# Optimization experiments

Measured on AMD Instinct MI355X. Metric: run time of the kernel, lower is better.

## Reference

```python
import jax, jax.numpy as jnp
import numpy as np
import math

DIM = 1024
N_HEADS = 16
HEAD_DIM = DIM // N_HEADS


def setup_inputs() -> dict:
    key = jax.random.key(0)
    kx, kk, kq, kv = jax.random.split(key, 4)
    x = jax.random.normal(kx, (4, 2048, DIM), dtype=jnp.float32)
    # torch.rand -> uniform [0,1)
    wk = jax.random.uniform(kk, (N_HEADS, DIM, HEAD_DIM), dtype=jnp.float32)
    wq = jax.random.uniform(kq, (N_HEADS, DIM, HEAD_DIM), dtype=jnp.float32)
    wv = jax.random.uniform(kv, (N_HEADS, DIM, HEAD_DIM), dtype=jnp.float32)
    return {"x": x, "wk": wk, "wq": wq, "wv": wv}


def reference(x, wk, wq, wv):
    # x: [b, l, d]; w*: [n, d, e]
    k = jnp.einsum('bld,nde->bnle', x, wk)
    q = jnp.einsum('bld,nde->bnle', x, wq)
    v = jnp.einsum('bld,nde->bnle', x, wv)
    head_dim = k.shape[-1]
    scores = jnp.einsum('bnle,bnme->bnlm', q, k) / math.sqrt(head_dim)
    s = jax.nn.softmax(scores, axis=-1)
    r = jnp.einsum('bnlm,bnme->blne', s, v)  # [b, l, n, e]
    b, l, n, e = r.shape
    return r.reshape(b, l, n * e)
```

## Files before the change

### kernel.cpp

```cpp
#include <hip/hip_runtime.h>
#include <math.h>

#define DIMX   1024
#define NHEADS 16
#define HD     64
#define BATCH  4
#define SEQ    2048
#define NM     (BATCH * NHEADS * SEQ * HD)

typedef unsigned short ushort_t;
typedef __attribute__((ext_vector_type(8))) short bf16x8;
typedef __attribute__((ext_vector_type(4))) short bf16x4;
typedef __attribute__((ext_vector_type(4))) float f32x4;

#define MFMA16(a, b, c) __builtin_amdgcn_mfma_f32_16x16x32_bf16(a, b, c, 0, 0, 0)

#if __has_builtin(__builtin_amdgcn_mfma_f32_16x16x16bf16_1k)
#define MFMA_PV(a, b, c) __builtin_amdgcn_mfma_f32_16x16x16bf16_1k(a, b, c, 0, 0, 0)
#else
static __device__ __forceinline__ f32x4 mfma_pv_asm(bf16x4 a, bf16x4 b, f32x4 c) {
    asm("v_mfma_f32_16x16x16_bf16 %0, %1, %2, %0" : "+v"(c) : "v"(a), "v"(b));
    return c;
}
#define MFMA_PV(a, b, c) mfma_pv_asm(a, b, c)
#endif

__device__ __forceinline__ ushort_t f2bf(float x) {
    unsigned u = __float_as_uint(x);
    u += 0x7fffu + ((u >> 16) & 1u);
    return (ushort_t)(u >> 16);
}
__device__ __forceinline__ float bf2f(ushort_t h) {
    return __uint_as_float(((unsigned)h) << 16);
}

__device__ __forceinline__ unsigned pack_bf16_trunc(float lo, float hi) {
#if __has_builtin(__builtin_amdgcn_perm)
    return __builtin_amdgcn_perm(__float_as_uint(hi), __float_as_uint(lo), 0x07060302u);
#else
    return (__float_as_uint(lo) >> 16) | (__float_as_uint(hi) & 0xFFFF0000u);
#endif
}
__device__ __forceinline__ float trunc_bf(float x) {
    return __uint_as_float(__float_as_uint(x) & 0xFFFF0000u);
}

__device__ __forceinline__ float fast_exp2(float x) {
#if __has_builtin(__builtin_amdgcn_exp2f)
    return __builtin_amdgcn_exp2f(x);
#else
    return exp2f(x);
#endif
}

#define GLOAD_LDS16(g, l) \
    __builtin_amdgcn_global_load_lds((const __attribute__((address_space(1))) unsigned int*)(g), \
                                     (__attribute__((address_space(3))) unsigned int*)(l), 16, 0, 0)

__global__ __launch_bounds__(256) void convert_x(
    const float* __restrict__ x, ushort_t* __restrict__ Xh, ushort_t* __restrict__ Xl)
{
    int i = blockIdx.x * 256 + threadIdx.x;
    #pragma unroll
    for (int t = 0; t < 4; t++) {
        int idx = t * 524288 + i;
        f32x4 v = ((const f32x4*)x)[idx];
        ushort4 hi, lo;
        hi.x = f2bf(v[0]); lo.x = f2bf(v[0] - bf2f(hi.x));
        hi.y = f2bf(v[1]); lo.y = f2bf(v[1] - bf2f(hi.y));
        hi.z = f2bf(v[2]); lo.z = f2bf(v[2] - bf2f(hi.z));
        hi.w = f2bf(v[3]); lo.w = f2bf(v[3] - bf2f(hi.w));
        ((ushort4*)Xh)[idx] = hi;
        ((ushort4*)Xl)[idx] = lo;
    }
}

__global__ __launch_bounds__(256) void convert_w(
    const float* __restrict__ wk, const float* __restrict__ wq, const float* __restrict__ wv,
    ushort_t* __restrict__ Bqh, ushort_t* __restrict__ Bql, ushort_t* __restrict__ Bvh)
{
    __shared__ float Ts[64][65];
    const int bid = blockIdx.x;
    const int mat = bid >> 8;
    const int rem = bid & 255;
    const int n  = rem >> 4;
    const int dt = rem & 15;
    const float* w = (mat == 0) ? wq : (mat == 1) ? wk : wv;
    const int tid = threadIdx.x;

    #pragma unroll
    for (int t = 0; t < 16; t++) {
        int i = tid + t * 256;
        int r = i >> 6, e = i & 63;
        Ts[r][e] = w[((size_t)n * 1024 + dt * 64 + r) * 64 + e];
    }
    __syncthreads();
    #pragma unroll
    for (int t = 0; t < 16; t++) {
        int i = tid + t * 256;
        int e = i >> 6, r = i & 63;
        float v = Ts[r][e];
        ushort_t hi = f2bf(v);
        size_t o = (size_t)(n * 64 + e) * 1024 + dt * 64 + r;
        if (mat < 2) {
            Bqh[(size_t)mat * 1048576 + o] = hi;
            Bql[(size_t)mat * 1048576 + o] = f2bf(v - bf2f(hi));
        } else {
            Bvh[o] = hi;
        }
    }
}

__global__ __launch_bounds__(256) void proj_qk(
    const ushort_t* __restrict__ Xh, const ushort_t* __restrict__ Xl,
    const ushort_t* __restrict__ Bh, const ushort_t* __restrict__ Bl,
    float* __restrict__ Qf, ushort_t* __restrict__ Khi, ushort_t* __restrict__ Klo)
{
    __shared__ __align__(16) ushort_t Ah[128 * 64];
    __shared__ __align__(16) ushort_t Al[128 * 64];
    __shared__ __align__(16) ushort_t Bhs[128 * 64];
    __shared__ __align__(16) ushort_t Bls[128 * 64];

    const int mt = blockIdx.x, nt = blockIdx.y;
    const int tid = threadIdx.x;
    const int w = tid >> 6, lane = tid & 63, col = lane & 15, quad = lane >> 4;
    const int wm = w & 1, wn = w >> 1;

    f32x4 acc[4][4] = {};

    for (int kc = 0; kc < 1024; kc += 64) {
        __syncthreads();
        #pragma unroll
        for (int i = 0; i < 4; i++) {
            int s = (w * 4 + i) * 64 + lane;
            int r = s >> 3, j = s & 7, g = j ^ (r & 7);
            size_t aoff = (size_t)(mt * 128 + r) * 1024 + kc + g * 8;
            size_t boff = (size_t)(nt * 128 + r) * 1024 + kc + g * 8;
            GLOAD_LDS16(Xh + aoff, Ah  + (size_t)(w * 4 + i) * 512);
            GLOAD_LDS16(Xl + aoff, Al  + (size_t)(w * 4 + i) * 512);
            GLOAD_LDS16(Bh + boff, Bhs + (size_t)(w * 4 + i) * 512);
            GLOAD_LDS16(Bl + boff, Bls + (size_t)(w * 4 + i) * 512);
        }
        __syncthreads();
        #pragma unroll
        for (int kk = 0; kk < 2; kk++) {
            bf16x8 a_h[4], a_l[4], b_h[4], b_l[4];
            const int gi = kk * 4 + quad;
            #pragma unroll
            for (int t = 0; t < 4; t++) {
                int rA = wm * 64 + t * 16 + col;
                int jA = gi ^ (rA & 7);
                a_h[t] = *(const bf16x8*)&Ah[(rA * 8 + jA) * 8];
                a_l[t] = *(const bf16x8*)&Al[(rA * 8 + jA) * 8];
                int rB = wn * 64 + t * 16 + col;
                int jB = gi ^ (rB & 7);
                b_h[t] = *(const bf16x8*)&Bhs[(rB * 8 + jB) * 8];
                b_l[t] = *(const bf16x8*)&Bls[(rB * 8 + jB) * 8];
            }
            #pragma unroll
            for (int t = 0; t < 4; t++)
                #pragma unroll
                for (int u = 0; u < 4; u++) {
                    acc[t][u] = MFMA16(a_h[t], b_h[u], acc[t][u]);
                    acc[t][u] = MFMA16(a_l[t], b_h[u], acc[t][u]);
                    acc[t][u] = MFMA16(a_h[t], b_l[u], acc[t][u]);
                }
        }
    }

    const bool isQ = (nt < 8);
    #pragma unroll
    for (int t = 0; t < 4; t++) {
        #pragma unroll
        for (int u = 0; u < 4; u++) {
            int np = nt * 128 + wn * 64 + u * 16 + col;
            int head = (np >> 6) & 15, e = np & 63;
            #pragma unroll
            for (int rr = 0; rr < 4; rr++) {
                int mm = mt * 128 + wm * 64 + t * 16 + quad * 4 + rr;
                int bi = mm >> 11, l = mm & 2047;
                size_t base = (((size_t)bi * NHEADS + head) * SEQ + l) * HD + e;
                float v = acc[t][u][rr];
                if (isQ) {
                    Qf[base] = v;
                } else {
                    ushort_t hi = f2bf(v);
                    Khi[base] = hi;
                    Klo[base] = f2bf(v - bf2f(hi));
                }
            }
        }
    }
}

__global__ __launch_bounds__(256) void proj_v(
    const ushort_t* __restrict__ Wvh, const ushort_t* __restrict__ Xh,
    ushort_t* __restrict__ Vt)
{
    __shared__ __align__(16) ushort_t Ah[128 * 64];
    __shared__ __align__(16) ushort_t Bhs[128 * 64];

    const int mt = blockIdx.x, nt = blockIdx.y;
    const int tid = threadIdx.x;
    const int w = tid >> 6, lane = tid & 63, col = lane & 15, quad = lane >> 4;
    const int wm = w & 1, wn = w >> 1;

    f32x4 acc[4][4] = {};

    for (int kc = 0; kc < 1024; kc += 64) {
        __syncthreads();
        #pragma unroll
        for (int i = 0; i < 4; i++) {
            int s = (w * 4 + i) * 64 + lane;
            int r = s >> 3, j = s & 7, g = j ^ (r & 7);
            size_t aoff = (size_t)(mt * 128 + r) * 1024 + kc + g * 8;
            size_t boff = (size_t)(nt * 128 + r) * 1024 + kc + g * 8;
            GLOAD_LDS16(Wvh + aoff, Ah  + (size_t)(w * 4 + i) * 512);
            GLOAD_LDS16(Xh  + boff, Bhs + (size_t)(w * 4 + i) * 512);
        }
        __syncthreads();
        #pragma unroll
        for (int kk = 0; kk < 2; kk++) {
            bf16x8 a_h[4], b_h[4];
            const int gi = kk * 4 + quad;
            #pragma unroll
            for (int t = 0; t < 4; t++) {
                int rA = wm * 64 + t * 16 + col;
                a_h[t] = *(const bf16x8*)&Ah[(rA * 8 + (gi ^ (rA & 7))) * 8];
                int rB = wn * 64 + t * 16 + col;
                b_h[t] = *(const bf16x8*)&Bhs[(rB * 8 + (gi ^ (rB & 7))) * 8];
            }
            #pragma unroll
            for (int t = 0; t < 4; t++)
                #pragma unroll
                for (int u = 0; u < 4; u++)
                    acc[t][u] = MFMA16(a_h[t], b_h[u], acc[t][u]);
        }
    }

    #pragma unroll
    for (int t = 0; t < 4; t++) {
        #pragma unroll
        for (int rr = 0; rr < 4; rr++) {
            int ep = mt * 128 + wm * 64 + t * 16 + quad * 4 + rr;
            int head = ep >> 6, e = ep & 63;
            #pragma unroll
            for (int u = 0; u < 4; u++) {
                int lg = nt * 128 + wn * 64 + u * 16 + col;
                int bi = lg >> 11, l = lg & 2047;
                Vt[(((size_t)bi * NHEADS + head) * HD + e) * SEQ + l] = f2bf(acc[t][u][rr]);
            }
        }
    }
}

__global__ __launch_bounds__(256, 4) void attn_mfma_kernel(
    const float* __restrict__ Qf, const ushort_t* __restrict__ Khi,
    const ushort_t* __restrict__ Klo, const ushort_t* __restrict__ Vt,
    float* __restrict__ out)
{
    __shared__ __align__(16) ushort_t Khs[64 * 64];
    __shared__ __align__(16) ushort_t Kls[64 * 64];
    __shared__ __align__(16) ushort_t Vts[64 * 64];

    const int qt  = blockIdx.x;
    const int bn  = blockIdx.y;
    const int tid = threadIdx.x;
    const int w    = tid >> 6;
    const int lane = tid & 63;
    const int col  = lane & 15;
    const int quad = lane >> 4;

    const ushort_t* Kh_g = Khi + (size_t)bn * SEQ * HD;
    const ushort_t* Kl_g = Klo + (size_t)bn * SEQ * HD;
    const ushort_t* Vt_g = Vt  + (size_t)bn * HD * SEQ;

    union { bf16x8 v; short s[8]; } qh[2], ql[2];
    {
        const int qrow = qt * 64 + w * 16 + col;
        const float* qp = Qf + ((size_t)bn * SEQ + qrow) * HD;
        #pragma unroll
        for (int ks = 0; ks < 2; ks++) {
            float qv[8];
            f32x4 a = *(const f32x4*)(qp + ks * 32 + quad * 8);
            f32x4 b = *(const f32x4*)(qp + ks * 32 + quad * 8 + 4);
            qv[0]=a[0]; qv[1]=a[1]; qv[2]=a[2]; qv[3]=a[3];
            qv[4]=b[0]; qv[5]=b[1]; qv[6]=b[2]; qv[7]=b[3];
            #pragma unroll
            for (int j = 0; j < 8; j++) {
                float xsc = qv[j] * (0.125f * 1.44269504088896f);
                ushort_t hi = f2bf(xsc);
                ushort_t lo = f2bf(xsc - bf2f(hi));
                qh[ks].s[j] = (short)hi;
                ql[ks].s[j] = (short)lo;
            }
        }
    }

    f32x4 O[4] = {};
    float m_i = -1e30f;
    float L   = 0.f;

    for (int ch = 0; ch < 32; ch++) {
        __syncthreads();
        #pragma unroll
        for (int t = 0; t < 2; t++) {
            int G   = (w * 2 + t) * 64 + lane;
            int key = G >> 3;
            int blk = (G & 7) ^ (key & 7);
            size_t koff = (size_t)(ch * 64 + key) * HD + blk * 8;
            size_t voff = (size_t)key * SEQ + ch * 64 + blk * 8;
            GLOAD_LDS16(Kh_g + koff, Khs + (w * 2 + t) * 512);
            GLOAD_LDS16(Kl_g + koff, Kls + (w * 2 + t) * 512);
            GLOAD_LDS16(Vt_g + voff, Vts + (w * 2 + t) * 512);
        }
        __syncthreads();

        f32x4 St[4] = {};
        #pragma unroll
        for (int ks = 0; ks < 2; ks++) {
            #pragma unroll
            for (int t = 0; t < 4; t++) {
                int key = t * 16 + col;
                int g = key * 8 + ((ks * 4 + quad) ^ (key & 7));
                bf16x8 kh = *(const bf16x8*)&Khs[g * 8];
                bf16x8 kl = *(const bf16x8*)&Kls[g * 8];
                St[t] = MFMA16(kh, qh[ks].v, St[t]);
                St[t] = MFMA16(kh, ql[ks].v, St[t]);
                St[t] = MFMA16(kl, qh[ks].v, St[t]);
            }
        }

        bf16x4 vfrag[4][4];
        #pragma unroll
        for (int u = 0; u < 4; u++) {
            int rowbase = (u * 16 + col) * 64;
            #pragma unroll
            for (int t = 0; t < 4; t++) {
                int g = (t * 2 + (quad >> 1)) ^ (col & 7);
                vfrag[u][t] = *(const bf16x4*)&Vts[rowbase + g * 8 + (quad & 1) * 4];
            }
        }

        float mx = St[0][0];
        #pragma unroll
        for (int t = 0; t < 4; t++)
            #pragma unroll
            for (int r = 0; r < 4; r++) mx = fmaxf(mx, St[t][r]);
        mx = fmaxf(mx, __shfl_xor(mx, 16));
        mx = fmaxf(mx, __shfl_xor(mx, 32));
        float mnew = fmaxf(m_i, mx);
        float al   = fast_exp2(m_i - mnew);
        m_i = mnew;

        float psum = 0.f;
        bf16x4 pf[4];
        #pragma unroll
        for (int t = 0; t < 4; t++) {
            float p0 = fast_exp2(St[t][0] - mnew);
            float p1 = fast_exp2(St[t][1] - mnew);
            float p2 = fast_exp2(St[t][2] - mnew);
            float p3 = fast_exp2(St[t][3] - mnew);
            psum += trunc_bf(p0) + trunc_bf(p1) + trunc_bf(p2) + trunc_bf(p3);
            union { unsigned u[2]; bf16x4 v; } pk;
            pk.u[0] = pack_bf16_trunc(p0, p1);
            pk.u[1] = pack_bf16_trunc(p2, p3);
            pf[t] = pk.v;
        }
        L = L * al + psum;
        #pragma unroll
        for (int u = 0; u < 4; u++) {
            O[u][0] *= al; O[u][1] *= al;
            O[u][2] *= al; O[u][3] *= al;
        }
        #pragma unroll
        for (int t = 0; t < 4; t++)
            #pragma unroll
            for (int u = 0; u < 4; u++)
                O[u] = MFMA_PV(vfrag[u][t], pf[t], O[u]);
    }

    const int b = bn >> 4, n = bn & 15;
    {
        float Lr = L;
        Lr += __shfl_xor(Lr, 16);
        Lr += __shfl_xor(Lr, 32);
        float inv = 1.0f / Lr;
        int l = qt * 64 + w * 16 + col;
        size_t base = ((size_t)(b * SEQ + l)) * (NHEADS * HD) + n * HD;
        #pragma unroll
        for (int u = 0; u < 4; u++) {
            f32x4 o;
            o[0] = O[u][0] * inv; o[1] = O[u][1] * inv;
            o[2] = O[u][2] * inv; o[3] = O[u][3] * inv;
            *(f32x4*)&out[base + u * 16 + quad * 4] = o;
        }
    }
}

extern "C" void kernel_launch(void* const* d_in, const int* in_sizes, int n_in,
                              void* d_out, int out_size, void* d_ws, size_t ws_size,
                              hipStream_t stream) {
    const float* x  = (const float*)d_in[0];
    const float* wk = (const float*)d_in[1];
    const float* wq = (const float*)d_in[2];
    const float* wv = (const float*)d_in[3];
    float* out = (float*)d_out;

    ushort_t* Xh  = (ushort_t*)d_ws;
    ushort_t* Xl  = Xh + NM;
    ushort_t* Vt  = Xl;
    ushort_t* Bqh = Xl + NM;
    ushort_t* Bql = Bqh + 2097152;
    ushort_t* Bvh = Bql + 2097152;
    float*    Qf  = (float*)(Bvh + 1048576);
    ushort_t* Khi = (ushort_t*)(Qf + NM);
    ushort_t* Klo = Khi + NM;

    convert_x<<<2048, 256, 0, stream>>>(x, Xh, Xl);
    convert_w<<<768, 256, 0, stream>>>(wk, wq, wv, Bqh, Bql, Bvh);
    proj_qk<<<dim3(64, 16), 256, 0, stream>>>(Xh, Xl, Bqh, Bql, Qf, Khi, Klo);
    proj_v<<<dim3(8, 64), 256, 0, stream>>>(Bvh, Xh, Vt);
    attn_mfma_kernel<<<dim3(32, 64), 256, 0, stream>>>(Qf, Khi, Klo, Vt, out);
}
```

Measured before the change: 364.5 us.

## Double-buffer K/V tiles in LDS and skip negligible attention chunks

The attention loop now uses two LDS buffer sets. The global-to-LDS loads for the next 64-key chunk are issued before the current chunk is computed, so load latency overlaps with the MFMA work. It also adds a wave-wide test: if no score in the chunk comes within 30 (log2 units) of the running max, the V fragment reads, exp2, rescale and PV MFMAs are skipped. Doubling LDS use to 48KB per block may lower the number of resident blocks per CU. The skip drops contributions below about 2^-30 relative to the max, which is a small approximation.

```diff
diff --git a/kernel.cpp b/kernel.cpp
--- a/kernel.cpp
+++ b/kernel.cpp
@@ -259,9 +259,12 @@
     const ushort_t* __restrict__ Klo, const ushort_t* __restrict__ Vt,
     float* __restrict__ out)
 {
-    __shared__ __align__(16) ushort_t Khs[64 * 64];
-    __shared__ __align__(16) ushort_t Kls[64 * 64];
-    __shared__ __align__(16) ushort_t Vts[64 * 64];
+    __shared__ __align__(16) ushort_t Khs0[64 * 64];
+    __shared__ __align__(16) ushort_t Kls0[64 * 64];
+    __shared__ __align__(16) ushort_t Vts0[64 * 64];
+    __shared__ __align__(16) ushort_t Khs1[64 * 64];
+    __shared__ __align__(16) ushort_t Kls1[64 * 64];
+    __shared__ __align__(16) ushort_t Vts1[64 * 64];
 
     const int qt  = blockIdx.x;
     const int bn  = blockIdx.y;
@@ -301,84 +304,102 @@
     float m_i = -1e30f;
     float L   = 0.f;
 
-    for (int ch = 0; ch < 32; ch++) {
-        __syncthreads();
-        #pragma unroll
-        for (int t = 0; t < 2; t++) {
-            int G   = (w * 2 + t) * 64 + lane;
-            int key = G >> 3;
-            int blk = (G & 7) ^ (key & 7);
-            size_t koff = (size_t)(ch * 64 + key) * HD + blk * 8;
-            size_t voff = (size_t)key * SEQ + ch * 64 + blk * 8;
-            GLOAD_LDS16(Kh_g + koff, Khs + (w * 2 + t) * 512);
-            GLOAD_LDS16(Kl_g + koff, Kls + (w * 2 + t) * 512);
-            GLOAD_LDS16(Vt_g + voff, Vts + (w * 2 + t) * 512);
-        }
-        __syncthreads();
-
-        f32x4 St[4] = {};
-        #pragma unroll
-        for (int ks = 0; ks < 2; ks++) {
-            #pragma unroll
-            for (int t = 0; t < 4; t++) {
-                int key = t * 16 + col;
-                int g = key * 8 + ((ks * 4 + quad) ^ (key & 7));
-                bf16x8 kh = *(const bf16x8*)&Khs[g * 8];
-                bf16x8 kl = *(const bf16x8*)&Kls[g * 8];
-                St[t] = MFMA16(kh, qh[ks].v, St[t]);
-                St[t] = MFMA16(kh, ql[ks].v, St[t]);
-                St[t] = MFMA16(kl, qh[ks].v, St[t]);
-            }
-        }
-
-        bf16x4 vfrag[4][4];
-        #pragma unroll
-        for (int u = 0; u < 4; u++) {
-            int rowbase = (u * 16 + col) * 64;
-            #pragma unroll
-            for (int t = 0; t < 4; t++) {
-                int g = (t * 2 + (quad >> 1)) ^ (col & 7);
-                vfrag[u][t] = *(const bf16x4*)&Vts[rowbase + g * 8 + (quad & 1) * 4];
-            }
-        }
-
-        float mx = St[0][0];
-        #pragma unroll
-        for (int t = 0; t < 4; t++)
-            #pragma unroll
-            for (int r = 0; r < 4; r++) mx = fmaxf(mx, St[t][r]);
-        mx = fmaxf(mx, __shfl_xor(mx, 16));
-        mx = fmaxf(mx, __shfl_xor(mx, 32));
-        float mnew = fmaxf(m_i, mx);
-        float al   = fast_exp2(m_i - mnew);
-        m_i = mnew;
-
-        float psum = 0.f;
-        bf16x4 pf[4];
-        #pragma unroll
-        for (int t = 0; t < 4; t++) {
-            float p0 = fast_exp2(St[t][0] - mnew);
-            float p1 = fast_exp2(St[t][1] - mnew);
-            float p2 = fast_exp2(St[t][2] - mnew);
-            float p3 = fast_exp2(St[t][3] - mnew);
-            psum += trunc_bf(p0) + trunc_bf(p1) + trunc_bf(p2) + trunc_bf(p3);
-            union { unsigned u[2]; bf16x4 v; } pk;
-            pk.u[0] = pack_bf16_trunc(p0, p1);
-            pk.u[1] = pack_bf16_trunc(p2, p3);
-            pf[t] = pk.v;
-        }
-        L = L * al + psum;
-        #pragma unroll
-        for (int u = 0; u < 4; u++) {
-            O[u][0] *= al; O[u][1] *= al;
-            O[u][2] *= al; O[u][3] *= al;
-        }
-        #pragma unroll
-        for (int t = 0; t < 4; t++)
-            #pragma unroll
-            for (int u = 0; u < 4; u++)
-                O[u] = MFMA_PV(vfrag[u][t], pf[t], O[u]);
-    }
+#define STAGE(CH, KHD, KLD, VTD) do {                                         \
+    _Pragma("unroll")                                                         \
+    for (int t_ = 0; t_ < 2; t_++) {                                          \
+        int G_   = (w * 2 + t_) * 64 + lane;                                  \
+        int key_ = G_ >> 3;                                                   \
+        int blk_ = (G_ & 7) ^ (key_ & 7);                                     \
+        size_t koff_ = (size_t)((CH) * 64 + key_) * HD + blk_ * 8;            \
+        size_t voff_ = (size_t)key_ * SEQ + (CH) * 64 + blk_ * 8;             \
+        GLOAD_LDS16(Kh_g + koff_, (KHD) + (w * 2 + t_) * 512);                \
+        GLOAD_LDS16(Kl_g + koff_, (KLD) + (w * 2 + t_) * 512);                \
+        GLOAD_LDS16(Vt_g + voff_, (VTD) + (w * 2 + t_) * 512);                \
+    }                                                                         \
+} while (0)
+
+#define CHUNK_COMPUTE(KHS, KLS, VTS) do {                                     \
+    f32x4 St[4] = {};                                                         \
+    _Pragma("unroll")                                                         \
+    for (int ks = 0; ks < 2; ks++) {                                          \
+        _Pragma("unroll")                                                     \
+        for (int t = 0; t < 4; t++) {                                         \
+            int key = t * 16 + col;                                           \
+            int g = key * 8 + ((ks * 4 + quad) ^ (key & 7));                  \
+            bf16x8 kh = *(const bf16x8*)&(KHS)[g * 8];                        \
+            bf16x8 kl = *(const bf16x8*)&(KLS)[g * 8];                        \
+            St[t] = MFMA16(kh, qh[ks].v, St[t]);                              \
+            St[t] = MFMA16(kh, ql[ks].v, St[t]);                              \
+            St[t] = MFMA16(kl, qh[ks].v, St[t]);                              \
+        }                                                                     \
+    }                                                                         \
+    float mx = St[0][0];                                                      \
+    _Pragma("unroll")                                                         \
+    for (int t = 0; t < 4; t++)                                               \
+        _Pragma("unroll")                                                     \
+        for (int r = 0; r < 4; r++) mx = fmaxf(mx, St[t][r]);                 \
+    mx = fmaxf(mx, __shfl_xor(mx, 16));                                       \
+    mx = fmaxf(mx, __shfl_xor(mx, 32));                                       \
+    if (__any(mx > m_i - 30.0f)) {                                            \
+        float mnew = fmaxf(m_i, mx);                                          \
+        float al   = fast_exp2(m_i - mnew);                                   \
+        m_i = mnew;                                                           \
+        bf16x4 vfrag[4][4];                                                   \
+        _Pragma("unroll")                                                     \
+        for (int u = 0; u < 4; u++) {                                         \
+            int rowbase = (u * 16 + col) * 64;                                \
+            _Pragma("unroll")                                                 \
+            for (int t = 0; t < 4; t++) {                                     \
+                int g = (t * 2 + (quad >> 1)) ^ (col & 7);                    \
+                vfrag[u][t] = *(const bf16x4*)&(VTS)[rowbase + g * 8 + (quad & 1) * 4]; \
+            }                                                                 \
+        }                                                                     \
+        float psum = 0.f;                                                     \
+        bf16x4 pf[4];                                                         \
+        _Pragma("unroll")                                                     \
+        for (int t = 0; t < 4; t++) {                                         \
+            float p0 = fast_exp2(St[t][0] - mnew);                            \
+            float p1 = fast_exp2(St[t][1] - mnew);                            \
+            float p2 = fast_exp2(St[t][2] - mnew);                            \
+            float p3 = fast_exp2(St[t][3] - mnew);                            \
+            psum += trunc_bf(p0) + trunc_bf(p1) + trunc_bf(p2) + trunc_bf(p3);\
+            union { unsigned u[2]; bf16x4 v; } pk;                            \
+            pk.u[0] = pack_bf16_trunc(p0, p1);                                \
+            pk.u[1] = pack_bf16_trunc(p2, p3);                                \
+            pf[t] = pk.v;                                                     \
+        }                                                                     \
+        L = L * al + psum;                                                    \
+        _Pragma("unroll")                                                     \
+        for (int u = 0; u < 4; u++) {                                         \
+            O[u][0] *= al; O[u][1] *= al;                                     \
+            O[u][2] *= al; O[u][3] *= al;                                     \
+        }                                                                     \
+        _Pragma("unroll")                                                     \
+        for (int t = 0; t < 4; t++)                                           \
+            _Pragma("unroll")                                                 \
+            for (int u = 0; u < 4; u++)                                       \
+                O[u] = MFMA_PV(vfrag[u][t], pf[t], O[u]);                     \
+    }                                                                         \
+} while (0)
+
+    STAGE(0, Khs0, Kls0, Vts0);
+    __syncthreads();
+
+    for (int ch = 0; ch < 30; ch += 2) {
+        STAGE(ch + 1, Khs1, Kls1, Vts1);
+        CHUNK_COMPUTE(Khs0, Kls0, Vts0);
+        __syncthreads();
+        STAGE(ch + 2, Khs0, Kls0, Vts0);
+        CHUNK_COMPUTE(Khs1, Kls1, Vts1);
+        __syncthreads();
+    }
+    STAGE(31, Khs1, Kls1, Vts1);
+    CHUNK_COMPUTE(Khs0, Kls0, Vts0);
+    __syncthreads();
+    CHUNK_COMPUTE(Khs1, Kls1, Vts1);
+
+#undef STAGE
+#undef CHUNK_COMPUTE
 
     const int b = bn >> 4, n = bn & 15;
     {
```

Result: no change. 369.6 us (+1.4%).
